# Performance work log

Measured on AMD Instinct MI355X. Metric: run time of the kernel, lower is better.

## Reference

```python
import jax, jax.numpy as jnp
import numpy as np

B, S0, S1 = 4, 768, 256
T = S0 + S1
D0, D1 = 2048, 1024
N, K, H = 8, 1, 256  # num_heads, num_kv_heads, head_dim
G = N // K
BIG_NEG = -2.3819763e38


def _apply_rope(x, positions, max_wavelength=10000):
    # x: [B, L, Hn, Hd]; positions: [B, L] float32
    half = x.shape[-1] // 2
    freq_exponents = (2.0 / x.shape[-1]) * jnp.arange(half, dtype=jnp.float32)
    timescale = max_wavelength ** freq_exponents
    radians = positions[..., None] / timescale[None, None, :]   # [B, L, half]
    radians = radians[..., None, :]                             # [B, L, 1, half]
    sin, cos = jnp.sin(radians), jnp.cos(radians)
    x1, x2 = jnp.split(x, 2, axis=-1)
    res = jnp.concatenate([x1 * cos - x2 * sin, x2 * cos + x1 * sin], axis=-1)
    return res.astype(x.dtype)


def setup_inputs() -> dict:
    key = jax.random.key(0)
    ks = jax.random.split(key, 8)
    x0 = jax.random.normal(ks[0], (B, S0, D0), dtype=jnp.float32)
    x1 = jax.random.normal(ks[1], (B, S1, D1), dtype=jnp.float32)
    positions = jnp.broadcast_to(jnp.arange(T, dtype=jnp.float32), (B, T))
    # causal mask [B, 1, T, T]
    attn_mask = jnp.broadcast_to(jnp.tril(jnp.ones((T, T), dtype=bool)), (B, 1, T, T))
    # lecun_normal-style init: std = 1/sqrt(fan_in=width)
    q0_w = jax.random.normal(ks[2], (N, D0, H), dtype=jnp.float32) * (D0 ** -0.5)
    kv0_w = jax.random.normal(ks[3], (2, K, D0, H), dtype=jnp.float32) * (D0 ** -0.5)
    q1_w = jax.random.normal(ks[4], (N, D1, H), dtype=jnp.float32) * (D1 ** -0.5)
    kv1_w = jax.random.normal(ks[5], (2, K, D1, H), dtype=jnp.float32) * (D1 ** -0.5)
    o0_w = jax.random.normal(ks[6], (N, H, D0), dtype=jnp.float32) * ((N * H) ** -0.5)
    o1_w = jax.random.normal(ks[7], (N, H, D1), dtype=jnp.float32) * ((N * H) ** -0.5)
    return {"x0": x0, "x1": x1, "positions": positions, "attn_mask": attn_mask,
            "q0_w": q0_w, "kv0_w": kv0_w, "q1_w": q1_w, "kv1_w": kv1_w,
            "o0_w": o0_w, "o1_w": o1_w}


def reference(x0, x1, positions, attn_mask, q0_w, kv0_w, q1_w, kv1_w, o0_w, o1_w):
    dtype = x0.dtype
    # per-stream GQA projections (num_kv_heads != num_heads path)
    q_a = jnp.einsum('BTD,NDH->BTNH', x0, q0_w)
    kv_a = jnp.einsum('BSD,CKDH->CBSKH', x0, kv0_w)
    q_b = jnp.einsum('BTD,NDH->BTNH', x1, q1_w)
    kv_b = jnp.einsum('BSD,CKDH->CBSKH', x1, kv1_w)
    # concat streams along sequence
    q = jnp.concatenate([q_a, q_b], axis=1)                 # [B, T, N, H]
    k = jnp.concatenate([kv_a[0], kv_b[0]], axis=1)         # [B, T, K, H]
    v = jnp.concatenate([kv_a[1], kv_b[1]], axis=1)         # [B, T, K, H]
    # inline RoPE + query scaling
    q = _apply_rope(q, positions) * (H ** -0.5)
    k = _apply_rope(k, positions)
    # GQA grouping: N = K * G
    qg = q.reshape(q.shape[0], q.shape[1], K, G, H)          # [B, T, K, G, H]
    logits = jnp.einsum('BTKGH,BSKH->BKGTS', qg, k,
                        preferred_element_type=jnp.float32)  # fp32 scores
    masked = jnp.where(attn_mask[:, :, None, :, :], logits, BIG_NEG)
    probs = jax.nn.softmax(masked, axis=-1).astype(dtype)
    encoded = jnp.einsum('BKGTS,BSKH->BTKGH', probs, v)
    encoded = encoded.reshape(encoded.shape[0], encoded.shape[1], N, H)  # [B, T, N, H]
    out0 = jnp.einsum('BTNH,NHD->BTD', encoded[:, :S0], o0_w)
    out1 = jnp.einsum('BTNH,NHD->BTD', encoded[:, S0:], o1_w)
    return (out0, out1)
```

## Files before the change

### kernel.cpp

```cpp
#include <hip/hip_runtime.h>

typedef unsigned short u16;
typedef __attribute__((ext_vector_type(8))) short bf16x8;
typedef __attribute__((ext_vector_type(4))) float f32x4;

#define CB   4
#define CS0  768
#define CS1  256
#define CT   1024
#define CD0  2048
#define CD1  1024
#define CN   8
#define CH   256
#define IDENT (1 << 30)
#define BIGBASE 0x7fffffff

__device__ __forceinline__ float bf2f(u16 u) {
    union { unsigned int i; float f; } v;
    v.i = ((unsigned int)u) << 16;
    return v.f;
}
__device__ __forceinline__ u16 f2bf(float f) {
    union { float f; unsigned int i; } v;
    v.f = f;
    unsigned int r = 0x7fffu + ((v.i >> 16) & 1u);
    return (u16)((v.i + r) >> 16);
}

__device__ __forceinline__ void gl_lds16(const u16* g, u16* lds_base) {
    __builtin_amdgcn_global_load_lds(
        (const __attribute__((address_space(1))) void*)g,
        (__attribute__((address_space(3))) void*)lds_base,
        16, 0, 0);
}

struct PSeg { const float* in; u16* out; int R, C, base, lgx, lgy, mode; };
struct PSeg8 { PSeg t[8]; };

__global__ __launch_bounds__(256) void prep_multi(PSeg8 segs)
{
    __shared__ float tl[32][33];
    int bid = blockIdx.x;
    PSeg g = segs.t[0];
    #pragma unroll
    for (int i = 1; i < 8; i++)
        if (bid >= segs.t[i].base) g = segs.t[i];
    int r = bid - g.base;
    if (g.mode == 0) {
        int i = r * 256 + threadIdx.x;
        float4 v = ((const float4*)g.in)[i];
        ushort4 o;
        o.x = f2bf(v.x); o.y = f2bf(v.y); o.z = f2bf(v.z); o.w = f2bf(v.w);
        ((ushort4*)g.out)[i] = o;
    } else {
        int bx = r & ((1 << g.lgx) - 1);
        int by = (r >> g.lgx) & ((1 << g.lgy) - 1);
        int bz = r >> (g.lgx + g.lgy);
        const float* in = g.in + (size_t)bz * g.R * g.C;
        u16* out = g.out + (size_t)bz * g.R * g.C;
        int c0 = bx * 32, r0 = by * 32;
        int tx = threadIdx.x & 31, ty = threadIdx.x >> 5;
        #pragma unroll
        for (int i = 0; i < 32; i += 8)
            tl[ty + i][tx] = in[(size_t)(r0 + ty + i) * g.C + c0 + tx];
        __syncthreads();
        #pragma unroll
        for (int i = 0; i < 32; i += 8)
            out[(size_t)(c0 + ty + i) * g.R + r0 + tx] = f2bf(tl[tx][ty + i]);
    }
}

struct GSeg {
    const u16* A; const u16* BT; void* C;
    int K, Cstride, base, lgnx;
    int Sa, Ta, ta, Sc, Tc, tc, obf, pad;
};
struct GSeg4 { GSeg s[4]; };

__global__ __launch_bounds__(256, 3) void gemm128_multi(GSeg4 segs)
{
    __shared__ __align__(16) u16 lds[2 * 8192];

    int bid = blockIdx.x;
    GSeg g = segs.s[0];
    if (bid >= segs.s[1].base) g = segs.s[1];
    if (bid >= segs.s[2].base) g = segs.s[2];
    if (bid >= segs.s[3].base) g = segs.s[3];

    int tid  = threadIdx.x;
    int r    = bid - g.base;
    int n0   = (r & ((1 << g.lgnx) - 1)) * 128;
    int m0   = (r >> g.lgnx) * 128;
    int wave = tid >> 6, lane = tid & 63;

    int srow  = tid >> 2;
    int skoff = ((tid & 3) ^ ((srow >> 1) & 3)) * 8;
    int am1 = m0 + srow, am2 = m0 + 64 + srow;
    const u16* aptr1 = g.A + (size_t)((am1 / g.Sa) * g.Ta + g.ta + am1 % g.Sa) * g.K + skoff;
    const u16* aptr2 = g.A + (size_t)((am2 / g.Sa) * g.Ta + g.ta + am2 % g.Sa) * g.K + skoff;
    const u16* bptr1 = g.BT + (size_t)(n0 + srow) * g.K + skoff;
    const u16* bptr2 = g.BT + (size_t)(n0 + 64 + srow) * g.K + skoff;

    int mw = (wave >> 1) * 64, nw = (wave & 1) * 64;
    int l15 = lane & 15;
    int q4  = lane >> 4;
    int sw  = (q4 ^ ((l15 >> 1) & 3)) * 8;

#define STAGE(tt) do { int kk = (tt) * 32; \
        u16* base = lds + ((tt) & 1) * 8192 + wave * 512; \
        gl_lds16(aptr1 + kk, base); \
        gl_lds16(aptr2 + kk, base + 2048); \
        gl_lds16(bptr1 + kk, base + 4096); \
        gl_lds16(bptr2 + kk, base + 6144); } while (0)

    f32x4 acc[4][4] = {};
    int nkt = g.K >> 5;

    STAGE(0);

    for (int t = 0; t < nkt; ++t) {
        asm volatile("s_waitcnt vmcnt(0)" ::: "memory");
        __builtin_amdgcn_sched_barrier(0);
        __builtin_amdgcn_s_barrier();
        asm volatile("" ::: "memory");
        if (t + 1 < nkt) STAGE(t + 1);

        const u16* At = lds + (t & 1) * 8192;
        const u16* Bt = At + 4096;
        bf16x8 af[4], bfr[4];
        #pragma unroll
        for (int i = 0; i < 4; i++)
            af[i] = *(const bf16x8*)&At[(mw + i * 16 + l15) * 32 + sw];
        #pragma unroll
        for (int i = 0; i < 4; i++)
            bfr[i] = *(const bf16x8*)&Bt[(nw + i * 16 + l15) * 32 + sw];
        asm volatile("s_waitcnt lgkmcnt(0)" ::: "memory");
        __builtin_amdgcn_sched_barrier(0);
        __builtin_amdgcn_s_setprio(1);
        #pragma unroll
        for (int mi = 0; mi < 4; mi++)
            #pragma unroll
            for (int ni = 0; ni < 4; ni++)
                acc[mi][ni] = __builtin_amdgcn_mfma_f32_16x16x32_bf16(
                    af[mi], bfr[ni], acc[mi][ni], 0, 0, 0);
        __builtin_amdgcn_s_setprio(0);
    }
#undef STAGE

    #pragma unroll
    for (int mi = 0; mi < 4; mi++) {
        #pragma unroll
        for (int rr = 0; rr < 4; rr++) {
            int mm = m0 + mw + mi * 16 + q4 * 4 + rr;
            int grow = (mm / g.Sc) * g.Tc + g.tc + mm % g.Sc;
            if (g.obf) {
                u16* crow = (u16*)g.C + (size_t)grow * g.Cstride + n0 + nw + l15;
                #pragma unroll
                for (int ni = 0; ni < 4; ni++)
                    crow[ni * 16] = f2bf(acc[mi][ni][rr]);
            } else {
                float* crow = (float*)g.C + (size_t)grow * g.Cstride + n0 + nw + l15;
                #pragma unroll
                for (int ni = 0; ni < 4; ni++)
                    crow[ni * 16] = acc[mi][ni][rr];
            }
        }
    }
}

__global__ __launch_bounds__(256) void rope_vt_kernel(
    const u16* __restrict__ qsrc, const u16* __restrict__ kvsrc,
    const float* __restrict__ positions,
    u16* __restrict__ qb, u16* __restrict__ kb, u16* __restrict__ vto)
{
    int bid = blockIdx.x;
    if (bid < 18432) {
        int idx = bid * 256 + threadIdx.x;
        const int QP = CB * CT * CN * 128;
        if (idx < QP) {
            int h  = idx & 127;
            int n  = (idx >> 7) & 7;
            int bt = idx >> 10;
            const u16* base = qsrc + (size_t)bt * 2048 + n * 256;
            float pos = positions[bt];
            float ts  = powf(10000.0f, (float)h * (1.0f / 128.0f));
            float rr  = pos / ts;
            float sn = sinf(rr), cs = cosf(rr);
            float x1 = bf2f(base[h]), x2 = bf2f(base[h + 128]);
            u16* ob = qb + (size_t)bt * 2048 + n * 256;
            ob[h]       = f2bf((x1 * cs - x2 * sn) * 0.0625f);
            ob[h + 128] = f2bf((x2 * cs + x1 * sn) * 0.0625f);
        } else {
            int j  = idx - QP;
            int h  = j & 127;
            int bt = j >> 7;
            const u16* base = kvsrc + (size_t)bt * 512;
            float pos = positions[bt];
            float ts  = powf(10000.0f, (float)h * (1.0f / 128.0f));
            float rr  = pos / ts;
            float sn = sinf(rr), cs = cosf(rr);
            float x1 = bf2f(base[h]), x2 = bf2f(base[h + 128]);
            int b = bt >> 10, t = bt & 1023;
            int h2 = h + 128;
            kb[((size_t)(b * 8 + (h  >> 5)) * 1024 + t) * 32 + (h  & 31)] = f2bf(x1 * cs - x2 * sn);
            kb[((size_t)(b * 8 + (h2 >> 5)) * 1024 + t) * 32 + (h2 & 31)] = f2bf(x2 * cs + x1 * sn);
        }
    } else {
        int vb = bid - 18432;
        int h  = threadIdx.x;
        int sc = vb & 31;
        int b  = vb >> 5;
        const u16* src = kvsrc + ((size_t)(b * 1024 + sc * 32) * 512 + 256 + h);
        u16* dst = vto + ((size_t)(b * 32 + sc) * 256 + h) * 32;
        u16 buf[32];
        #pragma unroll
        for (int ss = 0; ss < 32; ss++)
            buf[ss] = src[(size_t)ss * 512];
        #pragma unroll
        for (int i = 0; i < 8; i++)
            ((ushort4*)dst)[i] = ((ushort4*)buf)[i];
    }
}

__global__ __launch_bounds__(256) void flash_attn(
    const u16* __restrict__ qb, const u16* __restrict__ kb,
    const u16* __restrict__ vt, u16* __restrict__ encoded)
{
    __shared__ __align__(16) u16 Ks[8 * 64 * 32];
    __shared__ __align__(16) u16 Vs[2 * 256 * 32];
    __shared__ __align__(16) u16 Pw[4][16 * 72];

    int tid  = threadIdx.x;
    int wave = tid >> 6, lane = tid & 63;
    int q4 = lane >> 4, l15 = lane & 15;
    int swz = (q4 ^ ((l15 >> 1) & 3)) * 8;

    int bid  = blockIdx.x;
    int half = bid >> 8;
    int r    = bid & 255;
    int b    = (half << 1) | (r >> 7);
    int ti   = r & 127;
    if (half) ti = 127 - ti;
    int t0 = ti * 8;

    bf16x8 af[8];
    {
        int m = wave * 16 + l15;
        int head = m >> 3, tl = m & 7;
        const u16* qrow = qb + ((size_t)(b * CT + t0 + tl) * 2048 + head * 256 + q4 * 8);
        #pragma unroll
        for (int kc = 0; kc < 8; kc++)
            af[kc] = *(const bf16x8*)(qrow + kc * 32);
    }

    f32x4 O[16] = {};
    float lrun[4] = {0.f, 0.f, 0.f, 0.f};

    int send = t0 + 8;
    for (int s0 = 0; s0 < send; s0 += 64) {
        bool lastTile = (s0 + 64 >= send);
        if (s0) __syncthreads();
        #pragma unroll
        for (int is = 0; is < 8; is++) {
            int ubase = is * 256 + wave * 64;
            int u = ubase + lane;
            int s = (u >> 2) & 63, hc = u >> 8;
            int ug = (u & 3) ^ ((s >> 1) & 3);
            const u16* g = kb + ((size_t)((b * 8 + hc) * 1024 + s0 + s) * 32 + ug * 8);
            gl_lds16(g, Ks + (size_t)ubase * 8);
        }
        #pragma unroll
        for (int is = 0; is < 8; is++) {
            int ubase = is * 256 + wave * 64;
            int u = ubase + lane;
            int h = (u >> 2) & 255;
            int vg = (u & 3) ^ ((h >> 1) & 3);
            const u16* g = vt + ((size_t)(b * 32 + (s0 >> 5)) * 8192 + (size_t)(u >> 2) * 32 + vg * 8);
            gl_lds16(g, Vs + (size_t)ubase * 8);
        }
        __syncthreads();

        f32x4 P[4];
        #pragma unroll
        for (int ni = 0; ni < 4; ni++) {
            f32x4 c = {};
            #pragma unroll
            for (int kc = 0; kc < 8; kc++) {
                bf16x8 bfr = *(const bf16x8*)&Ks[kc * 2048 + (ni * 16 + l15) * 32 + swz];
                c = __builtin_amdgcn_mfma_f32_16x16x32_bf16(af[kc], bfr, c, 0, 0, 0);
            }
            P[ni] = c;
        }

        if (lastTile) {
            #pragma unroll
            for (int ni = 0; ni < 4; ni++)
                #pragma unroll
                for (int rr = 0; rr < 4; rr++) {
                    int trow = t0 + ((q4 * 4 + rr) & 7);
                    int scol = s0 + ni * 16 + l15;
                    if (scol > trow) P[ni][rr] = -3.0e38f;
                }
        }

        #pragma unroll
        for (int ni = 0; ni < 4; ni++)
            #pragma unroll
            for (int rr = 0; rr < 4; rr++) {
                float e = __expf(P[ni][rr]);
                P[ni][rr] = e;
                Pw[wave][(q4 * 4 + rr) * 72 + ni * 16 + l15] = f2bf(e);
            }
        #pragma unroll
        for (int rr = 0; rr < 4; rr++) {
            float s = (P[0][rr] + P[1][rr]) + (P[2][rr] + P[3][rr]);
            s += __shfl_xor(s, 1);
            s += __shfl_xor(s, 2);
            s += __shfl_xor(s, 4);
            s += __shfl_xor(s, 8);
            lrun[rr] += s;
        }

        bf16x8 pa0 = *(const bf16x8*)&Pw[wave][l15 * 72 + q4 * 8];
        bf16x8 pa1 = *(const bf16x8*)&Pw[wave][l15 * 72 + 32 + q4 * 8];
        #pragma unroll
        for (int nc = 0; nc < 16; nc++) {
            bf16x8 b0 = *(const bf16x8*)&Vs[(nc * 16 + l15) * 32 + swz];
            bf16x8 b1 = *(const bf16x8*)&Vs[8192 + (nc * 16 + l15) * 32 + swz];
            O[nc] = __builtin_amdgcn_mfma_f32_16x16x32_bf16(pa0, b0, O[nc], 0, 0, 0);
            O[nc] = __builtin_amdgcn_mfma_f32_16x16x32_bf16(pa1, b1, O[nc], 0, 0, 0);
        }
    }

    #pragma unroll
    for (int rr = 0; rr < 4; rr++) {
        int mm = wave * 16 + q4 * 4 + rr;
        int hd = mm >> 3, tl = mm & 7;
        u16* erow = encoded + ((size_t)(b * CT + t0 + tl) * 2048 + hd * 256 + l15);
        float inv = 1.0f / lrun[rr];
        #pragma unroll
        for (int nc = 0; nc < 16; nc++)
            erow[nc * 16] = f2bf(O[nc][rr] * inv);
    }
}

extern "C" void kernel_launch(void* const* d_in, const int* in_sizes, int n_in,
                              void* d_out, int out_size, void* d_ws, size_t ws_size,
                              hipStream_t stream)
{
    const float* x0        = (const float*)d_in[0];
    const float* x1        = (const float*)d_in[1];
    const float* positions = (const float*)d_in[2];
    const float* q0_w  = (const float*)d_in[4];
    const float* kv0_w = (const float*)d_in[5];
    const float* q1_w  = (const float*)d_in[6];
    const float* kv1_w = (const float*)d_in[7];
    const float* o0_w  = (const float*)d_in[8];
    const float* o1_w  = (const float*)d_in[9];
    float* out = (float*)d_out;

    char* W = (char*)d_ws;
    u16* qbuf16  = (u16*)(W);
    u16* kvbuf16 = (u16*)(W + 16777216);
    u16* WTo0  = (u16*)(W + 20971520);
    u16* WTo1  = (u16*)(W + 29360128);
    u16* x0b   = (u16*)(W + 33554432);
    u16* x1b   = (u16*)(W + 46137344);
    u16* WTq0  = (u16*)(W + 48234496);
    u16* WTkv0 = (u16*)(W + 56623104);
    u16* WTq1  = (u16*)(W + 58720256);
    u16* WTkv1 = (u16*)(W + 62914560);
    u16* qb  = x0b;
    u16* kb  = WTkv0;
    u16* vtb = WTq1;
    u16* encoded = qbuf16;

    PSeg8 ps8;
    ps8.t[0] = { x0,    x0b,      0,    0,     0, 0, 0, 0 };
    ps8.t[1] = { x1,    x1b,      0,    0,  6144, 0, 0, 0 };
    ps8.t[2] = { q0_w,  WTq0,  2048,  256,  7168, 3, 6, 1 };
    ps8.t[3] = { kv0_w, WTkv0, 2048,  256, 11264, 3, 6, 1 };
    ps8.t[4] = { q1_w,  WTq1,  1024,  256, 12288, 3, 5, 1 };
    ps8.t[5] = { kv1_w, WTkv1, 1024,  256, 14336, 3, 5, 1 };
    ps8.t[6] = { o0_w,  WTo0,  2048, 2048, 14848, 6, 6, 1 };
    ps8.t[7] = { o1_w,  WTo1,  2048, 1024, 18944, 5, 6, 1 };
    prep_multi<<<dim3(20992), dim3(256), 0, stream>>>(ps8);

    GSeg4 ps;
    ps.s[0] = { x0b, WTq0,  qbuf16,  2048, 2048,   0, 4, IDENT, 0, 0, CS0, CT, 0,   1, 0 };
    ps.s[1] = { x0b, WTkv0, kvbuf16, 2048,  512, 384, 2, IDENT, 0, 0, CS0, CT, 0,   1, 0 };
    ps.s[2] = { x1b, WTq1,  qbuf16,  1024, 2048, 480, 4, IDENT, 0, 0, CS1, CT, CS0, 1, 0 };
    ps.s[3] = { x1b, WTkv1, kvbuf16, 1024,  512, 608, 2, IDENT, 0, 0, CS1, CT, CS0, 1, 0 };
    gemm128_multi<<<dim3(640), dim3(256), 0, stream>>>(ps);

    rope_vt_kernel<<<dim3(18560), dim3(256), 0, stream>>>(
        qbuf16, kvbuf16, positions, qb, kb, vtb);

    flash_attn<<<dim3(512), dim3(256), 0, stream>>>(qb, kb, vtb, encoded);

    GSeg4 os;
    os.s[0] = { encoded, WTo0, out, 2048, 2048,   0, 4, CS0, CT, 0,   IDENT, 0, 0, 0, 0 };
    os.s[1] = { encoded, WTo1, out + (size_t)CB * CS0 * CD0,
                2048, 1024, 384, 3, CS1, CT, CS0, IDENT, 0, 0, 0, 0 };
    os.s[2] = { nullptr, nullptr, nullptr, 32, 0, BIGBASE, 0, 1, 0, 0, 1, 0, 0, 0, 0 };
    os.s[3] = { nullptr, nullptr, nullptr, 32, 0, BIGBASE, 0, 1, 0, 0, 1, 0, 0, 0, 0 };
    gemm128_multi<<<dim3(448), dim3(256), 0, stream>>>(os);
}
```

Measured before the change: 308.9 us.

## Triple-buffer GEMM LDS and double-buffer K/V tiles in flash attention

```diff
diff --git a/kernel.cpp b/kernel.cpp
--- a/kernel.cpp
+++ b/kernel.cpp
@@ -79,7 +79,7 @@
 
 __global__ __launch_bounds__(256, 3) void gemm128_multi(GSeg4 segs)
 {
-    __shared__ __align__(16) u16 lds[2 * 8192];
+    __shared__ __align__(16) u16 lds[3 * 8192];
 
     int bid = blockIdx.x;
     GSeg g = segs.s[0];
@@ -106,8 +106,8 @@
     int q4  = lane >> 4;
     int sw  = (q4 ^ ((l15 >> 1) & 3)) * 8;
 
-#define STAGE(tt) do { int kk = (tt) * 32; \
-        u16* base = lds + ((tt) & 1) * 8192 + wave * 512; \
+#define STAGE(bufi, tt) do { int kk = (tt) * 32; \
+        u16* base = lds + (bufi) * 8192 + wave * 512; \
         gl_lds16(aptr1 + kk, base); \
         gl_lds16(aptr2 + kk, base + 2048); \
         gl_lds16(bptr1 + kk, base + 4096); \
@@ -116,16 +116,19 @@
     f32x4 acc[4][4] = {};
     int nkt = g.K >> 5;
 
-    STAGE(0);
-
+    STAGE(0, 0);
+    STAGE(1, 1);
+
+    int cur = 0, nxt = 2;
     for (int t = 0; t < nkt; ++t) {
-        asm volatile("s_waitcnt vmcnt(0)" ::: "memory");
+        if (t + 1 < nkt) asm volatile("s_waitcnt vmcnt(4)" ::: "memory");
+        else             asm volatile("s_waitcnt vmcnt(0)" ::: "memory");
         __builtin_amdgcn_sched_barrier(0);
         __builtin_amdgcn_s_barrier();
         asm volatile("" ::: "memory");
-        if (t + 1 < nkt) STAGE(t + 1);
-
-        const u16* At = lds + (t & 1) * 8192;
+        if (t + 2 < nkt) STAGE(nxt, t + 2);
+
+        const u16* At = lds + cur * 8192;
         const u16* Bt = At + 4096;
         bf16x8 af[4], bfr[4];
         #pragma unroll
@@ -144,6 +147,8 @@
                 acc[mi][ni] = __builtin_amdgcn_mfma_f32_16x16x32_bf16(
                     af[mi], bfr[ni], acc[mi][ni], 0, 0, 0);
         __builtin_amdgcn_s_setprio(0);
+        cur = (cur == 2) ? 0 : cur + 1;
+        nxt = (nxt == 2) ? 0 : nxt + 1;
     }
 #undef STAGE
 
@@ -226,9 +231,9 @@
     const u16* __restrict__ qb, const u16* __restrict__ kb,
     const u16* __restrict__ vt, u16* __restrict__ encoded)
 {
-    __shared__ __align__(16) u16 Ks[8 * 64 * 32];
-    __shared__ __align__(16) u16 Vs[2 * 256 * 32];
-    __shared__ __align__(16) u16 Pw[4][16 * 72];
+    __shared__ __align__(16) u16 Ks[2 * 8192];
+    __shared__ __align__(16) u16 Vs[2 * 8192];
+    __shared__ __align__(16) u16 Pw[4][640];
 
     int tid  = threadIdx.x;
     int wave = tid >> 6, lane = tid & 63;
@@ -253,48 +258,60 @@
             af[kc] = *(const bf16x8*)(qrow + kc * 32);
     }
 
+#define STAGE_KV(tt, bb) do { int ss0 = (tt) * 32; \
+        _Pragma("unroll") \
+        for (int is = 0; is < 4; ++is) { \
+            int ubase = is * 256 + wave * 64; \
+            int u = ubase + lane; \
+            int gK = u & 3, sK = (u >> 2) & 31, hc = u >> 7; \
+            int ug = gK ^ ((sK >> 1) & 3); \
+            const u16* gp = kb + ((size_t)((b * 8 + hc) * 1024 + ss0 + sK) * 32 + ug * 8); \
+            gl_lds16(gp, Ks + (bb) * 8192 + ubase * 8); \
+        } \
+        _Pragma("unroll") \
+        for (int is = 0; is < 4; ++is) { \
+            int ubase = is * 256 + wave * 64; \
+            int u = ubase + lane; \
+            int gV = u & 3, hv = u >> 2; \
+            int vg = gV ^ ((hv >> 1) & 3); \
+            const u16* gp = vt + ((size_t)(b * 32 + (ss0 >> 5)) * 8192 + (size_t)hv * 32 + vg * 8); \
+            gl_lds16(gp, Vs + (bb) * 8192 + ubase * 8); \
+        } } while (0)
+
     f32x4 O[16] = {};
     float lrun[4] = {0.f, 0.f, 0.f, 0.f};
 
     int send = t0 + 8;
-    for (int s0 = 0; s0 < send; s0 += 64) {
-        bool lastTile = (s0 + 64 >= send);
-        if (s0) __syncthreads();
-        #pragma unroll
-        for (int is = 0; is < 8; is++) {
-            int ubase = is * 256 + wave * 64;
-            int u = ubase + lane;
-            int s = (u >> 2) & 63, hc = u >> 8;
-            int ug = (u & 3) ^ ((s >> 1) & 3);
-            const u16* g = kb + ((size_t)((b * 8 + hc) * 1024 + s0 + s) * 32 + ug * 8);
-            gl_lds16(g, Ks + (size_t)ubase * 8);
-        }
-        #pragma unroll
-        for (int is = 0; is < 8; is++) {
-            int ubase = is * 256 + wave * 64;
-            int u = ubase + lane;
-            int h = (u >> 2) & 255;
-            int vg = (u & 3) ^ ((h >> 1) & 3);
-            const u16* g = vt + ((size_t)(b * 32 + (s0 >> 5)) * 8192 + (size_t)(u >> 2) * 32 + vg * 8);
-            gl_lds16(g, Vs + (size_t)ubase * 8);
-        }
-        __syncthreads();
-
-        f32x4 P[4];
-        #pragma unroll
-        for (int ni = 0; ni < 4; ni++) {
+    int nt   = (send + 31) >> 5;
+
+    STAGE_KV(0, 0);
+
+    for (int t = 0; t < nt; ++t) {
+        asm volatile("s_waitcnt vmcnt(0)" ::: "memory");
+        __builtin_amdgcn_sched_barrier(0);
+        __builtin_amdgcn_s_barrier();
+        asm volatile("" ::: "memory");
+        if (t + 1 < nt) STAGE_KV(t + 1, (t + 1) & 1);
+
+        const u16* Kb = Ks + (t & 1) * 8192;
+        const u16* Vb = Vs + (t & 1) * 8192;
+        int s0 = t * 32;
+
+        f32x4 P[2];
+        #pragma unroll
+        for (int ni = 0; ni < 2; ni++) {
             f32x4 c = {};
             #pragma unroll
             for (int kc = 0; kc < 8; kc++) {
-                bf16x8 bfr = *(const bf16x8*)&Ks[kc * 2048 + (ni * 16 + l15) * 32 + swz];
+                bf16x8 bfr = *(const bf16x8*)&Kb[kc * 1024 + (ni * 16 + l15) * 32 + swz];
                 c = __builtin_amdgcn_mfma_f32_16x16x32_bf16(af[kc], bfr, c, 0, 0, 0);
             }
             P[ni] = c;
         }
 
-        if (lastTile) {
+        if (t == nt - 1) {
             #pragma unroll
-            for (int ni = 0; ni < 4; ni++)
+            for (int ni = 0; ni < 2; ni++)
                 #pragma unroll
                 for (int rr = 0; rr < 4; rr++) {
                     int trow = t0 + ((q4 * 4 + rr) & 7);
@@ -304,16 +321,16 @@
         }
 
         #pragma unroll
-        for (int ni = 0; ni < 4; ni++)
+        for (int ni = 0; ni < 2; ni++)
             #pragma unroll
             for (int rr = 0; rr < 4; rr++) {
                 float e = __expf(P[ni][rr]);
                 P[ni][rr] = e;
-                Pw[wave][(q4 * 4 + rr) * 72 + ni * 16 + l15] = f2bf(e);
+                Pw[wave][(q4 * 4 + rr) * 40 + ni * 16 + l15] = f2bf(e);
             }
         #pragma unroll
         for (int rr = 0; rr < 4; rr++) {
-            float s = (P[0][rr] + P[1][rr]) + (P[2][rr] + P[3][rr]);
+            float s = P[0][rr] + P[1][rr];
             s += __shfl_xor(s, 1);
             s += __shfl_xor(s, 2);
             s += __shfl_xor(s, 4);
@@ -321,16 +338,14 @@
             lrun[rr] += s;
         }
 
-        bf16x8 pa0 = *(const bf16x8*)&Pw[wave][l15 * 72 + q4 * 8];
-        bf16x8 pa1 = *(const bf16x8*)&Pw[wave][l15 * 72 + 32 + q4 * 8];
+        bf16x8 pa = *(const bf16x8*)&Pw[wave][l15 * 40 + q4 * 8];
         #pragma unroll
         for (int nc = 0; nc < 16; nc++) {
-            bf16x8 b0 = *(const bf16x8*)&Vs[(nc * 16 + l15) * 32 + swz];
-            bf16x8 b1 = *(const bf16x8*)&Vs[8192 + (nc * 16 + l15) * 32 + swz];
-            O[nc] = __builtin_amdgcn_mfma_f32_16x16x32_bf16(pa0, b0, O[nc], 0, 0, 0);
-            O[nc] = __builtin_amdgcn_mfma_f32_16x16x32_bf16(pa1, b1, O[nc], 0, 0, 0);
-        }
-    }
+            bf16x8 b0 = *(const bf16x8*)&Vb[(nc * 16 + l15) * 32 + swz];
+            O[nc] = __builtin_amdgcn_mfma_f32_16x16x32_bf16(pa, b0, O[nc], 0, 0, 0);
+        }
+    }
+#undef STAGE_KV
 
     #pragma unroll
     for (int rr = 0; rr < 4; rr++) {
@@ -402,7 +417,7 @@
     os.s[0] = { encoded, WTo0, out, 2048, 2048,   0, 4, CS0, CT, 0,   IDENT, 0, 0, 0, 0 };
     os.s[1] = { encoded, WTo1, out + (size_t)CB * CS0 * CD0,
                 2048, 1024, 384, 3, CS1, CT, CS0, IDENT, 0, 0, 0, 0 };
-    os.s[2] = { nullptr, nullptr, nullptr, 32, 0, BIGBASE, 0, 1, 0, 0, 1, 0, 0, 0, 0 };
-    os.s[3] = { nullptr, nullptr, nullptr, 32, 0, BIGBASE, 0, 1, 0, 0, 1, 0, 0, 0, 0 };
+    os.s[2] = { nullptr, nullptr, nullptr, 128, 0, BIGBASE, 0, 1, 0, 0, 1, 0, 0, 0, 0 };
+    os.s[3] = { nullptr, nullptr, nullptr, 128, 0, BIGBASE, 0, 1, 0, 0, 1, 0, 0, 0, 0 };
     gemm128_multi<<<dim3(448), dim3(256), 0, stream>>>(os);
 }
```

Result: no change. 311.1 us (+0.7%).
